# Kernel optimization log

Hardware: AMD Instinct MI355X
Metric: run time of the kernel (lower is better)

Reference implementation:

```python
import jax, jax.numpy as jnp
import numpy as np

WINDOW = 14

def _make_rel_index(ws):
    coords = np.stack(np.meshgrid(np.arange(ws), np.arange(ws), indexing='ij'))  # [2,ws,ws]
    flat = coords.reshape(2, -1)
    rel = flat[:, :, None] - flat[:, None, :]            # [2,N,N]
    rel = rel.transpose(1, 2, 0).copy()
    rel[:, :, 0] += ws - 1
    rel[:, :, 1] += ws - 1
    rel[:, :, 0] *= 2 * ws - 1
    return rel.sum(-1).astype(np.int32)                  # [N,N]

def setup_inputs() -> dict:
    key = jax.random.key(0)
    ks = jax.random.split(key, 7)
    B, N, C, H = 256, WINDOW * WINDOW, 768, 12
    s = 0.02
    return {
        'x': jax.random.normal(ks[0], (B, N, C), jnp.float32),
        'qkv_w': jax.random.normal(ks[1], (3 * C, C), jnp.float32) * s,
        'q_bias': jnp.zeros((C,), jnp.float32),
        'v_bias': jnp.zeros((C,), jnp.float32),
        'rpb_table': jax.random.normal(ks[2], ((2 * WINDOW - 1) ** 2, H), jnp.float32) * s,
        'proj_w': jax.random.normal(ks[3], (C, C), jnp.float32) * s,
        'proj_b': jnp.zeros((C,), jnp.float32),
        'rel_index': jnp.asarray(_make_rel_index(WINDOW)),
        'num_heads': H,
    }

def reference(x, qkv_w, q_bias, v_bias, rpb_table, proj_w, proj_b, rel_index, num_heads):
    B, N, C = x.shape
    H = num_heads
    hd = C // H
    scale = hd ** -0.5
    qkv_bias = jnp.concatenate([q_bias, jnp.zeros_like(v_bias), v_bias])
    qkv = x @ qkv_w.T + qkv_bias                          # [B,N,3C]
    qkv = qkv.reshape(B, N, 3, H, hd).transpose(2, 0, 3, 1, 4)  # [3,B,H,N,hd]
    q, k, v = qkv[0] * scale, qkv[1], qkv[2]
    attn = jnp.einsum('bhnd,bhmd->bhnm', q, k)            # [B,H,N,N]
    rpb = rpb_table[rel_index.reshape(-1)].reshape(N, N, H).transpose(2, 0, 1)  # [H,N,N]
    attn = jax.nn.softmax(attn + rpb, axis=-1)
    out = jnp.einsum('bhnm,bhmd->bhnd', attn, v)          # [B,H,N,hd]
    out = out.transpose(0, 2, 1, 3).reshape(B, N, C)
    return out @ proj_w.T + proj_b
```

## Files before the change

kernel.cpp:

```cpp
#include <hip/hip_runtime.h>
#include <hip/hip_fp16.h>

typedef _Float16 f16;
typedef __attribute__((ext_vector_type(4))) _Float16 f16x4;
typedef __attribute__((ext_vector_type(8))) _Float16 f16x8;
typedef __attribute__((ext_vector_type(4))) float f32x4;

#define MFMA16 __builtin_amdgcn_mfma_f32_16x16x32_f16
#define BAR() __builtin_amdgcn_s_barrier()
#define VMCNT(n) asm volatile("s_waitcnt vmcnt(" #n ")" ::: "memory")
#define LGKM(n) asm volatile("s_waitcnt lgkmcnt(" #n ")" ::: "memory")
#define SCHEDB() __builtin_amdgcn_sched_barrier(0)

__device__ __forceinline__ void gload16(const f16* g, char* l) {
  __builtin_amdgcn_global_load_lds(
      (const __attribute__((address_space(1))) void*)g,
      (__attribute__((address_space(3))) void*)l, 16, 0, 0);
}

__global__ __launch_bounds__(256) void cvt_k(const float* __restrict__ in,
                                             f16* __restrict__ out, int n8) {
  int i = blockIdx.x * 256 + threadIdx.x;
  const int stride = gridDim.x * 256;
  for (; i < n8; i += stride) {
    const f32x4* p = (const f32x4*)(in + (size_t)i * 8);
    f32x4 a = __builtin_nontemporal_load(p);
    f32x4 b = __builtin_nontemporal_load(p + 1);
    f16x8 h;
    h[0] = (f16)a[0]; h[1] = (f16)a[1]; h[2] = (f16)a[2]; h[3] = (f16)a[3];
    h[4] = (f16)b[0]; h[5] = (f16)b[1]; h[6] = (f16)b[2]; h[7] = (f16)b[3];
    *(f16x8*)(out + (size_t)i * 8) = h;
  }
}

__global__ __launch_bounds__(256) void rpb_build_k(const float* __restrict__ tab,
                                                   const int* __restrict__ rel,
                                                   f16* __restrict__ out) {
  int i = blockIdx.x * 256 + threadIdx.x;
  if (i >= 196 * 196) return;
  int idx = __builtin_nontemporal_load(rel + i);
#pragma unroll
  for (int h = 0; h < 12; ++h)
    out[h * (196 * 196) + i] = (f16)tab[idx * 12 + h];
}

template <int MODE>
__global__ __launch_bounds__(512) void gemm_k(
    const f16* __restrict__ A, const f16* __restrict__ W,
    const float* __restrict__ bias_a, const float* __restrict__ bias_b,
    f16* __restrict__ q_out, f16* __restrict__ k_out, f16* __restrict__ vT_out,
    float* __restrict__ f_out) {
  constexpr int NTIL = (MODE == 0) ? 9 : 3;
  constexpr int NWG = 196 * NTIL;
  constexpr int QX = NWG / 8, RX = NWG % 8;
  constexpr int KT = 12;

  extern __shared__ char lds[];

  const int tid = threadIdx.x;
  const int lane = tid & 63, wid = tid >> 6;
  const int xcd = blockIdx.x & 7, bix = blockIdx.x >> 3;
  const int lbid =
      (xcd < RX ? xcd * (QX + 1) : RX * (QX + 1) + (xcd - RX) * QX) + bix;
  const int bcol = lbid / 196, brow = lbid % 196;
  const int wr = wid >> 2, wc = wid & 3;
  const int l15 = lane & 15, g4 = lane >> 4;

  const int sr = wid * 8 + (lane >> 3);
  const int scw = ((lane & 7) ^ (lane >> 3)) * 8;
  const f16* pAt = A + (size_t)(brow * 256 + sr) * 768 + scw;
  const f16* pBt = W + (size_t)(bcol * 256 + sr) * 768 + scw;
  char* ldsW = lds + wid * 1024;

  auto stA = [&](int kt) {
    char* base = ldsW + (kt % 3) * 32768;
#pragma unroll
    for (int i = 0; i < 4; ++i)
      gload16(pAt + (size_t)(i * 64) * 768 + kt * 64, base + i * 8192);
  };
  auto stB = [&](int kt) {
    char* base = ldsW + 98304 + (kt & 1) * 32768;
#pragma unroll
    for (int i = 0; i < 4; ++i)
      gload16(pBt + (size_t)(i * 64) * 768 + kt * 64, base + i * 8192);
  };

  f16x8 af[2][4][2], bf[2][2][2];
  const int aswz = l15 & 7;
  const char* ldsAl = lds + (size_t)(wr * 128 + l15) * 128;
  const char* ldsBl = lds + 98304 + (size_t)(wc * 64 + l15) * 128;

  auto rdA = [&](int q, int t) {
    const char* b = ldsAl + (t % 3) * 32768;
#pragma unroll
    for (int mf = 0; mf < 4; ++mf)
#pragma unroll
      for (int ks = 0; ks < 2; ++ks)
        af[q][mf][ks] = *(const f16x8*)(b + (q * 64 + mf * 16) * 128 +
                                        ((ks * 4 + g4) ^ aswz) * 16);
  };
  auto rdB = [&](int r, int t) {
    const char* b = ldsBl + (t & 1) * 32768;
#pragma unroll
    for (int nf = 0; nf < 2; ++nf)
#pragma unroll
      for (int ks = 0; ks < 2; ++ks)
        bf[r][nf][ks] = *(const f16x8*)(b + (r * 32 + nf * 16) * 128 +
                                        ((ks * 4 + g4) ^ aswz) * 16);
  };

  const f32x4 zero4 = {0.f, 0.f, 0.f, 0.f};
  f32x4 acc[8][4];
#pragma unroll
  for (int i = 0; i < 8; ++i)
#pragma unroll
    for (int j = 0; j < 4; ++j) acc[i][j] = zero4;

  auto mm = [&](int q, int r) {
#pragma unroll
    for (int ks = 0; ks < 2; ++ks)
#pragma unroll
      for (int mf = 0; mf < 4; ++mf)
#pragma unroll
        for (int nf = 0; nf < 2; ++nf)
          acc[q * 4 + mf][r * 2 + nf] =
              MFMA16(af[q][mf][ks], bf[r][nf][ks], acc[q * 4 + mf][r * 2 + nf],
                     0, 0, 0);
  };

  stA(0); stB(0); stA(1);

  for (int t = 0; t < KT; ++t) {
    if (t == KT - 1) { VMCNT(0); } else { VMCNT(4); }
    BAR();
    if (t + 1 < KT) stB(t + 1);
    if (t + 2 < KT) stA(t + 2);
    rdA(0, t); rdB(0, t);
    SCHEDB();
    rdA(1, t); rdB(1, t);
    LGKM(12);
    SCHEDB();
    __builtin_amdgcn_s_setprio(1); mm(0, 0); mm(0, 1); __builtin_amdgcn_s_setprio(0);
    LGKM(0);
    SCHEDB();
    __builtin_amdgcn_s_setprio(1); mm(1, 0); mm(1, 1); __builtin_amdgcn_s_setprio(0);
  }

  if constexpr (MODE == 0) {
    const int s = bcol / 3;
#pragma unroll
    for (int mf = 0; mf < 8; ++mf) {
      const int rowo = wr * 128 + (mf >> 2) * 64 + (mf & 3) * 16 + g4 * 4;
      const int grow0 = brow * 256 + rowo;
      const int bI = grow0 / 196;
      const int nI0 = grow0 - bI * 196;
#pragma unroll
      for (int nf = 0; nf < 4; ++nf) {
        const int col = bcol * 256 + wc * 64 + (nf >> 1) * 32 + (nf & 1) * 16 + l15;
        const int rem = col - s * 768;
        const int hh = rem >> 6, dd = rem & 63;
        if (s == 2) {
          f16x4 vv;
#pragma unroll
          for (int rr = 0; rr < 4; ++rr)
            vv[rr] = (f16)(acc[mf][nf][rr] + bias_b[rem]);
          *(f16x4*)(vT_out + (((size_t)bI * 12 + hh) * 64 + dd) * 224 + nI0) = vv;
        } else if (s == 0) {
#pragma unroll
          for (int rr = 0; rr < 4; ++rr) {
            float v = (acc[mf][nf][rr] + bias_a[rem]) * 0.125f;
            q_out[(((size_t)bI * 12 + hh) * 196 + nI0 + rr) * 64 + dd] = (f16)v;
          }
        } else {
#pragma unroll
          for (int rr = 0; rr < 4; ++rr)
            k_out[(((size_t)bI * 12 + hh) * 196 + nI0 + rr) * 64 + dd] =
                (f16)acc[mf][nf][rr];
        }
      }
    }
  } else {
#pragma unroll
    for (int mf = 0; mf < 8; ++mf) {
      const int rowo = wr * 128 + (mf >> 2) * 64 + (mf & 3) * 16 + g4 * 4;
#pragma unroll
      for (int rr = 0; rr < 4; ++rr) {
        const int grow = brow * 256 + rowo + rr;
        float* orow = f_out + (size_t)grow * 768;
#pragma unroll
        for (int nf = 0; nf < 4; ++nf) {
          const int col = bcol * 256 + wc * 64 + (nf >> 1) * 32 + (nf & 1) * 16 + l15;
          orow[col] = acc[mf][nf][rr] + bias_a[col];
        }
      }
    }
  }
}

__global__ __launch_bounds__(256) void attn_k(const f16* __restrict__ qg,
                                              const f16* __restrict__ kg,
                                              const f16* __restrict__ vTg,
                                              const f16* __restrict__ rpb,
                                              f16* __restrict__ og) {
  extern __shared__ char smem[];
  f16x8* Vlds = (f16x8*)smem;
  f16x8* Plds = (f16x8*)(smem + 32768);

  const int tid = threadIdx.x;
  const int bh = blockIdx.x;
  const int b = bh / 12, h = bh - b * 12;
  const int lane = tid & 63, wid = tid >> 6;
  const int l15 = lane & 15, g4 = lane >> 4;

  f16x8 z8;
#pragma unroll
  for (int j = 0; j < 8; ++j) z8[j] = (f16)0.f;

  const f16* vgb = vTg + (size_t)bh * (64 * 224);
  for (int c = tid; c < 64 * 32; c += 256) {
    int d = c >> 5, mc = c & 31;
    f16x8 v;
    if (mc < 24) {
      v = *(const f16x8*)(vgb + d * 224 + mc * 8);
    } else if (mc == 24) {
      v = *(const f16x8*)(vgb + d * 224 + mc * 8);
#pragma unroll
      for (int j = 4; j < 8; ++j) v[j] = (f16)0.f;
    } else {
      v = z8;
    }
    Vlds[d * 32 + (mc ^ (d & 7))] = v;
  }
  f16x8* Pw = Plds + wid * (16 * 32);
  if (g4 < 2) {
    int n = l15;
    Pw[n * 32 + ((26 + g4) ^ (n & 7))] = z8;
  }
  __syncthreads();

  const f16* qgb = qg + (size_t)bh * (196 * 64);
  const f16* kgb = kg + (size_t)bh * (196 * 64);
  const f16* rpbh = rpb + (size_t)h * (196 * 196);

  for (int rt = wid; rt < 13; rt += 4) {
    const int n0 = rt * 16;
    f16x8 qf0 = *(const f16x8*)(qgb + (n0 + l15) * 64 + g4 * 8);
    f16x8 qf1 = *(const f16x8*)(qgb + (n0 + l15) * 64 + 32 + g4 * 8);

    float rv[13][4];
#pragma unroll
    for (int mt = 0; mt < 13; ++mt) {
      const int m = mt * 16 + l15;
      const int mcl = (m < 196) ? m : 195;
#pragma unroll
      for (int r = 0; r < 4; ++r) {
        const int n = n0 + g4 * 4 + r;
        const int ncl = (n < 196) ? n : 195;
        rv[mt][r] = (float)rpbh[ncl * 196 + mcl];
      }
    }

    const f32x4 zero4 = {0.f, 0.f, 0.f, 0.f};
    f32x4 s[13];
#pragma unroll
    for (int mt = 0; mt < 13; ++mt) {
      const int m = mt * 16 + l15;
      f16x8 k0 = *(const f16x8*)(kgb + m * 64 + g4 * 8);
      f16x8 k1 = *(const f16x8*)(kgb + m * 64 + 32 + g4 * 8);
      s[mt] = MFMA16(qf0, k0, zero4, 0, 0, 0);
      s[mt] = MFMA16(qf1, k1, s[mt], 0, 0, 0);
    }

    float mx[4] = {-3e38f, -3e38f, -3e38f, -3e38f};
#pragma unroll
    for (int mt = 0; mt < 13; ++mt) {
      const int m = mt * 16 + l15;
#pragma unroll
      for (int r = 0; r < 4; ++r) {
        const int n = n0 + g4 * 4 + r;
        float v = (m < 196 && n < 196) ? s[mt][r] + rv[mt][r] : -1e30f;
        s[mt][r] = v;
        mx[r] = fmaxf(mx[r], v);
      }
    }
#pragma unroll
    for (int r = 0; r < 4; ++r) {
      mx[r] = fmaxf(mx[r], __shfl_xor(mx[r], 1));
      mx[r] = fmaxf(mx[r], __shfl_xor(mx[r], 2));
      mx[r] = fmaxf(mx[r], __shfl_xor(mx[r], 4));
      mx[r] = fmaxf(mx[r], __shfl_xor(mx[r], 8));
    }
    float sm[4] = {0.f, 0.f, 0.f, 0.f};
#pragma unroll
    for (int mt = 0; mt < 13; ++mt)
#pragma unroll
      for (int r = 0; r < 4; ++r) {
        float p = __expf(s[mt][r] - mx[r]);
        s[mt][r] = p;
        sm[r] += p;
      }
#pragma unroll
    for (int r = 0; r < 4; ++r) {
      sm[r] += __shfl_xor(sm[r], 1);
      sm[r] += __shfl_xor(sm[r], 2);
      sm[r] += __shfl_xor(sm[r], 4);
      sm[r] += __shfl_xor(sm[r], 8);
    }
    float rinv[4];
#pragma unroll
    for (int r = 0; r < 4; ++r) rinv[r] = 1.f / sm[r];

#pragma unroll
    for (int mt = 0; mt < 13; ++mt) {
      const int m = mt * 16 + l15;
#pragma unroll
      for (int r = 0; r < 4; ++r) {
        const int n = g4 * 4 + r;
        f16* dst = (f16*)Pw + n * 256 + (((m >> 3) ^ (n & 7)) << 3) + (m & 7);
        *dst = (f16)s[mt][r];
      }
    }

    f32x4 o[4];
#pragma unroll
    for (int dt = 0; dt < 4; ++dt) o[dt] = zero4;
#pragma unroll
    for (int ks = 0; ks < 7; ++ks) {
      f16x8 pa = Pw[l15 * 32 + ((ks * 4 + g4) ^ (l15 & 7))];
#pragma unroll
      for (int dt = 0; dt < 4; ++dt) {
        const int d = dt * 16 + l15;
        f16x8 vf = Vlds[d * 32 + ((ks * 4 + g4) ^ (d & 7))];
        o[dt] = MFMA16(pa, vf, o[dt], 0, 0, 0);
      }
    }

#pragma unroll
    for (int r = 0; r < 4; ++r) {
      const int n = n0 + g4 * 4 + r;
      if (n < 196) {
        f16* orow = og + ((size_t)b * 196 + n) * 768 + h * 64;
#pragma unroll
        for (int dt = 0; dt < 4; ++dt)
          orow[dt * 16 + l15] = (f16)(o[dt][r] * rinv[r]);
      }
    }
  }
}

extern "C" void kernel_launch(void* const* d_in, const int* in_sizes, int n_in,
                              void* d_out, int out_size, void* d_ws, size_t ws_size,
                              hipStream_t stream) {
  const float* x = (const float*)d_in[0];
  const float* qkv_w = (const float*)d_in[1];
  const float* q_bias = (const float*)d_in[2];
  const float* v_bias = (const float*)d_in[3];
  const float* rpb_tab = (const float*)d_in[4];
  const float* proj_w = (const float*)d_in[5];
  const float* proj_b = (const float*)d_in[6];
  const int* rel = (const int*)d_in[7];
  float* out = (float*)d_out;

  const size_t SZ_Q = 77070336;
  const size_t SZ_K = 77070336;
  const size_t SZ_VT = 88080384;
  const size_t SZ_AO = 77070336;
  const size_t SZ_RP = 921984;
  const size_t SZ_WQ = 3538944;
  const size_t SZ_WP = 1179648;
  if (ws_size < SZ_Q + SZ_K + SZ_VT + SZ_AO + SZ_RP + SZ_WQ + SZ_WP) return;

  char* w = (char*)d_ws;
  f16* q_ = (f16*)w;
  f16* k_ = (f16*)(w + SZ_Q);
  f16* vT_ = (f16*)(w + SZ_Q + SZ_K);
  f16* ao_ = (f16*)(w + SZ_Q + SZ_K + SZ_VT);
  f16* rp_ = (f16*)(w + SZ_Q + SZ_K + SZ_VT + SZ_AO);
  f16* whq_ = (f16*)(w + SZ_Q + SZ_K + SZ_VT + SZ_AO + SZ_RP);
  f16* whp_ = (f16*)(w + SZ_Q + SZ_K + SZ_VT + SZ_AO + SZ_RP + SZ_WQ);
  f16* xh_ = ao_;

  (void)hipFuncSetAttribute((const void*)attn_k,
                            hipFuncAttributeMaxDynamicSharedMemorySize, 65536);
  (void)hipFuncSetAttribute((const void*)gemm_k<0>,
                            hipFuncAttributeMaxDynamicSharedMemorySize, 163840);
  (void)hipFuncSetAttribute((const void*)gemm_k<1>,
                            hipFuncAttributeMaxDynamicSharedMemorySize, 163840);

  cvt_k<<<2048, 256, 0, stream>>>(x, xh_, 50176 * 768 / 8);
  cvt_k<<<864, 256, 0, stream>>>(qkv_w, whq_, 2304 * 768 / 8);
  cvt_k<<<288, 256, 0, stream>>>(proj_w, whp_, 768 * 768 / 8);
  rpb_build_k<<<(196 * 196 + 255) / 256, 256, 0, stream>>>(rpb_tab, rel, rp_);

  gemm_k<0><<<1764, 512, 163840, stream>>>(xh_, whq_, q_bias, v_bias,
                                           q_, k_, vT_, nullptr);
  attn_k<<<3072, 256, 65536, stream>>>(q_, k_, vT_, rp_, ao_);
  gemm_k<1><<<588, 512, 163840, stream>>>(ao_, whp_, proj_b, nullptr,
                                          nullptr, nullptr, nullptr, out);
}
```

Measured before the change: 663.1 us.

## Keep softmax probabilities in registers and prepack bias as MFMA accumulator init

The attention kernel now computes S^T (K as the A operand), so each lane holds a full column of scores. A prepacked fp32 bias tensor in MFMA fragment layout, with -1e30 masking baked in, seeds the accumulator directly. Softmax reductions drop to two cross-lane shuffles, and P is normalized before the PV product. P reaches the PV MFMA through register shuffles instead of LDS, which halves LDS use and allows four blocks per CU. The bias pack is built after the QKV GEMM, reusing the qkv weight buffer, and the extra shuffles and fp32 bias reads add cost.

```diff
diff --git a/kernel.cpp b/kernel.cpp
--- a/kernel.cpp
+++ b/kernel.cpp
@@ -5,6 +5,8 @@
 typedef __attribute__((ext_vector_type(4))) _Float16 f16x4;
 typedef __attribute__((ext_vector_type(8))) _Float16 f16x8;
 typedef __attribute__((ext_vector_type(4))) float f32x4;
+typedef __attribute__((ext_vector_type(2))) unsigned int u32x2;
+typedef __attribute__((ext_vector_type(4))) unsigned int u32x4;
 
 #define MFMA16 __builtin_amdgcn_mfma_f32_16x16x32_f16
 #define BAR() __builtin_amdgcn_s_barrier()
@@ -33,15 +35,23 @@
   }
 }
 
-__global__ __launch_bounds__(256) void rpb_build_k(const float* __restrict__ tab,
-                                                   const int* __restrict__ rel,
-                                                   f16* __restrict__ out) {
-  int i = blockIdx.x * 256 + threadIdx.x;
-  if (i >= 196 * 196) return;
-  int idx = __builtin_nontemporal_load(rel + i);
-#pragma unroll
-  for (int h = 0; h < 12; ++h)
-    out[h * (196 * 196) + i] = (f16)tab[idx * 12 + h];
+__global__ __launch_bounds__(256) void rpb_pack_k(const float* __restrict__ tab,
+                                                  const int* __restrict__ rel,
+                                                  f32x4* __restrict__ pack) {
+  int idx = blockIdx.x * 256 + threadIdx.x;
+  if (idx >= 12 * 169 * 64) return;
+  const int lane = idx & 63, t = idx >> 6;
+  const int h = t / 169, rem = t - h * 169;
+  const int rt = rem / 13, mt = rem - rt * 13;
+  const int l15 = lane & 15, g4 = lane >> 4;
+  const int n = rt * 16 + l15;
+  f32x4 v;
+#pragma unroll
+  for (int r = 0; r < 4; ++r) {
+    const int m = mt * 16 + g4 * 4 + r;
+    v[r] = (n < 196 && m < 196) ? tab[rel[n * 196 + m] * 12 + h] : -1e30f;
+  }
+  pack[(size_t)t * 64 + lane] = v;
 }
 
 template <int MODE>
@@ -197,14 +207,13 @@
   }
 }
 
-__global__ __launch_bounds__(256) void attn_k(const f16* __restrict__ qg,
-                                              const f16* __restrict__ kg,
-                                              const f16* __restrict__ vTg,
-                                              const f16* __restrict__ rpb,
-                                              f16* __restrict__ og) {
+__global__ __launch_bounds__(256, 4) void attn_k(const f16* __restrict__ qg,
+                                                 const f16* __restrict__ kg,
+                                                 const f16* __restrict__ vTg,
+                                                 const f32x4* __restrict__ pack,
+                                                 f16* __restrict__ og) {
   extern __shared__ char smem[];
   f16x8* Vlds = (f16x8*)smem;
-  f16x8* Plds = (f16x8*)(smem + 32768);
 
   const int tid = threadIdx.x;
   const int bh = blockIdx.x;
@@ -231,102 +240,83 @@
     }
     Vlds[d * 32 + (mc ^ (d & 7))] = v;
   }
-  f16x8* Pw = Plds + wid * (16 * 32);
-  if (g4 < 2) {
-    int n = l15;
-    Pw[n * 32 + ((26 + g4) ^ (n & 7))] = z8;
-  }
   __syncthreads();
 
   const f16* qgb = qg + (size_t)bh * (196 * 64);
   const f16* kgb = kg + (size_t)bh * (196 * 64);
-  const f16* rpbh = rpb + (size_t)h * (196 * 196);
+  const f32x4* packh = pack + (size_t)h * 169 * 64;
 
   for (int rt = wid; rt < 13; rt += 4) {
     const int n0 = rt * 16;
     f16x8 qf0 = *(const f16x8*)(qgb + (n0 + l15) * 64 + g4 * 8);
     f16x8 qf1 = *(const f16x8*)(qgb + (n0 + l15) * 64 + 32 + g4 * 8);
-
-    float rv[13][4];
-#pragma unroll
-    for (int mt = 0; mt < 13; ++mt) {
-      const int m = mt * 16 + l15;
-      const int mcl = (m < 196) ? m : 195;
-#pragma unroll
-      for (int r = 0; r < 4; ++r) {
-        const int n = n0 + g4 * 4 + r;
-        const int ncl = (n < 196) ? n : 195;
-        rv[mt][r] = (float)rpbh[ncl * 196 + mcl];
-      }
-    }
-
-    const f32x4 zero4 = {0.f, 0.f, 0.f, 0.f};
+    const f32x4* pt = packh + rt * 13 * 64 + lane;
+
     f32x4 s[13];
 #pragma unroll
     for (int mt = 0; mt < 13; ++mt) {
       const int m = mt * 16 + l15;
       f16x8 k0 = *(const f16x8*)(kgb + m * 64 + g4 * 8);
       f16x8 k1 = *(const f16x8*)(kgb + m * 64 + 32 + g4 * 8);
-      s[mt] = MFMA16(qf0, k0, zero4, 0, 0, 0);
-      s[mt] = MFMA16(qf1, k1, s[mt], 0, 0, 0);
-    }
-
-    float mx[4] = {-3e38f, -3e38f, -3e38f, -3e38f};
+      f32x4 ci = pt[mt * 64];
+      s[mt] = MFMA16(k0, qf0, ci, 0, 0, 0);
+      s[mt] = MFMA16(k1, qf1, s[mt], 0, 0, 0);
+    }
+
+    float mx = -3e38f;
+#pragma unroll
+    for (int mt = 0; mt < 13; ++mt)
+#pragma unroll
+      for (int r = 0; r < 4; ++r) mx = fmaxf(mx, s[mt][r]);
+    mx = fmaxf(mx, __shfl_xor(mx, 16));
+    mx = fmaxf(mx, __shfl_xor(mx, 32));
+    float sm = 0.f;
+#pragma unroll
+    for (int mt = 0; mt < 13; ++mt)
+#pragma unroll
+      for (int r = 0; r < 4; ++r) {
+        float p = __expf(s[mt][r] - mx);
+        s[mt][r] = p;
+        sm += p;
+      }
+    sm += __shfl_xor(sm, 16);
+    sm += __shfl_xor(sm, 32);
+    const float rinv = 1.f / sm;
+
+    unsigned pkl[14], pkh[14];
 #pragma unroll
     for (int mt = 0; mt < 13; ++mt) {
-      const int m = mt * 16 + l15;
-#pragma unroll
-      for (int r = 0; r < 4; ++r) {
-        const int n = n0 + g4 * 4 + r;
-        float v = (m < 196 && n < 196) ? s[mt][r] + rv[mt][r] : -1e30f;
-        s[mt][r] = v;
-        mx[r] = fmaxf(mx[r], v);
-      }
-    }
-#pragma unroll
-    for (int r = 0; r < 4; ++r) {
-      mx[r] = fmaxf(mx[r], __shfl_xor(mx[r], 1));
-      mx[r] = fmaxf(mx[r], __shfl_xor(mx[r], 2));
-      mx[r] = fmaxf(mx[r], __shfl_xor(mx[r], 4));
-      mx[r] = fmaxf(mx[r], __shfl_xor(mx[r], 8));
-    }
-    float sm[4] = {0.f, 0.f, 0.f, 0.f};
-#pragma unroll
-    for (int mt = 0; mt < 13; ++mt)
-#pragma unroll
-      for (int r = 0; r < 4; ++r) {
-        float p = __expf(s[mt][r] - mx[r]);
-        s[mt][r] = p;
-        sm[r] += p;
-      }
-#pragma unroll
-    for (int r = 0; r < 4; ++r) {
-      sm[r] += __shfl_xor(sm[r], 1);
-      sm[r] += __shfl_xor(sm[r], 2);
-      sm[r] += __shfl_xor(sm[r], 4);
-      sm[r] += __shfl_xor(sm[r], 8);
-    }
-    float rinv[4];
-#pragma unroll
-    for (int r = 0; r < 4; ++r) rinv[r] = 1.f / sm[r];
-
-#pragma unroll
-    for (int mt = 0; mt < 13; ++mt) {
-      const int m = mt * 16 + l15;
-#pragma unroll
-      for (int r = 0; r < 4; ++r) {
-        const int n = g4 * 4 + r;
-        f16* dst = (f16*)Pw + n * 256 + (((m >> 3) ^ (n & 7)) << 3) + (m & 7);
-        *dst = (f16)s[mt][r];
-      }
-    }
-
+      f16x4 hv;
+#pragma unroll
+      for (int r = 0; r < 4; ++r) hv[r] = (f16)(s[mt][r] * rinv);
+      u32x2 u = __builtin_bit_cast(u32x2, hv);
+      pkl[mt] = u[0];
+      pkh[mt] = u[1];
+    }
+    pkl[13] = 0u; pkh[13] = 0u;
+
+    const f32x4 zero4 = {0.f, 0.f, 0.f, 0.f};
     f32x4 o[4];
 #pragma unroll
     for (int dt = 0; dt < 4; ++dt) o[dt] = zero4;
+    const int srcA = l15 + ((g4 & 1) << 5);
+    const bool hi = (g4 & 2);
 #pragma unroll
     for (int ks = 0; ks < 7; ++ks) {
-      f16x8 pa = Pw[l15 * 32 + ((ks * 4 + g4) ^ (l15 & 7))];
+      unsigned e0 = __shfl(pkl[2 * ks], srcA);
+      unsigned f0 = __shfl(pkl[2 * ks + 1], srcA);
+      unsigned e1 = __shfl(pkh[2 * ks], srcA);
+      unsigned f1 = __shfl(pkh[2 * ks + 1], srcA);
+      unsigned e2 = __shfl(pkl[2 * ks], srcA + 16);
+      unsigned f2 = __shfl(pkl[2 * ks + 1], srcA + 16);
+      unsigned e3 = __shfl(pkh[2 * ks], srcA + 16);
+      unsigned f3 = __shfl(pkh[2 * ks + 1], srcA + 16);
+      u32x4 t;
+      t[0] = hi ? f0 : e0;
+      t[1] = hi ? f1 : e1;
+      t[2] = hi ? f2 : e2;
+      t[3] = hi ? f3 : e3;
+      f16x8 pa = __builtin_bit_cast(f16x8, t);
 #pragma unroll
       for (int dt = 0; dt < 4; ++dt) {
         const int d = dt * 16 + l15;
@@ -342,7 +332,7 @@
         f16* orow = og + ((size_t)b * 196 + n) * 768 + h * 64;
 #pragma unroll
         for (int dt = 0; dt < 4; ++dt)
-          orow[dt * 16 + l15] = (f16)(o[dt][r] * rinv[r]);
+          orow[dt * 16 + l15] = (f16)o[dt][r];
       }
     }
   }
@@ -365,23 +355,22 @@
   const size_t SZ_K = 77070336;
   const size_t SZ_VT = 88080384;
   const size_t SZ_AO = 77070336;
-  const size_t SZ_RP = 921984;
   const size_t SZ_WQ = 3538944;
   const size_t SZ_WP = 1179648;
-  if (ws_size < SZ_Q + SZ_K + SZ_VT + SZ_AO + SZ_RP + SZ_WQ + SZ_WP) return;
+  if (ws_size < SZ_Q + SZ_K + SZ_VT + SZ_AO + SZ_WQ + SZ_WP) return;
 
   char* w = (char*)d_ws;
   f16* q_ = (f16*)w;
   f16* k_ = (f16*)(w + SZ_Q);
   f16* vT_ = (f16*)(w + SZ_Q + SZ_K);
   f16* ao_ = (f16*)(w + SZ_Q + SZ_K + SZ_VT);
-  f16* rp_ = (f16*)(w + SZ_Q + SZ_K + SZ_VT + SZ_AO);
-  f16* whq_ = (f16*)(w + SZ_Q + SZ_K + SZ_VT + SZ_AO + SZ_RP);
-  f16* whp_ = (f16*)(w + SZ_Q + SZ_K + SZ_VT + SZ_AO + SZ_RP + SZ_WQ);
+  f16* whq_ = (f16*)(w + SZ_Q + SZ_K + SZ_VT + SZ_AO);
+  f16* whp_ = (f16*)(w + SZ_Q + SZ_K + SZ_VT + SZ_AO + SZ_WQ);
   f16* xh_ = ao_;
+  f32x4* pack_ = (f32x4*)whq_;
 
   (void)hipFuncSetAttribute((const void*)attn_k,
-                            hipFuncAttributeMaxDynamicSharedMemorySize, 65536);
+                            hipFuncAttributeMaxDynamicSharedMemorySize, 32768);
   (void)hipFuncSetAttribute((const void*)gemm_k<0>,
                             hipFuncAttributeMaxDynamicSharedMemorySize, 163840);
   (void)hipFuncSetAttribute((const void*)gemm_k<1>,
@@ -390,11 +379,11 @@
   cvt_k<<<2048, 256, 0, stream>>>(x, xh_, 50176 * 768 / 8);
   cvt_k<<<864, 256, 0, stream>>>(qkv_w, whq_, 2304 * 768 / 8);
   cvt_k<<<288, 256, 0, stream>>>(proj_w, whp_, 768 * 768 / 8);
-  rpb_build_k<<<(196 * 196 + 255) / 256, 256, 0, stream>>>(rpb_tab, rel, rp_);
 
   gemm_k<0><<<1764, 512, 163840, stream>>>(xh_, whq_, q_bias, v_bias,
                                            q_, k_, vT_, nullptr);
-  attn_k<<<3072, 256, 65536, stream>>>(q_, k_, vT_, rp_, ao_);
+  rpb_pack_k<<<507, 256, 0, stream>>>(rpb_tab, rel, pack_);
+  attn_k<<<3072, 256, 32768, stream>>>(q_, k_, vT_, pack_, ao_);
   gemm_k<1><<<588, 512, 163840, stream>>>(ao_, whp_, proj_b, nullptr,
                                           nullptr, nullptr, nullptr, out);
 }
```

Result: slower. 932.2 us (+40.6%).
